# Kernel tuning notes

Hardware: AMD Instinct MI355X
Metric: run time of the kernel (lower is better)

## Reference

```python
import jax, jax.numpy as jnp
import numpy as np

N = 100000
E = 1600000
D_IN = 128
D_OUT = 128
BN_EPS = 1e-5


def setup_inputs() -> dict:
    key = jax.random.key(0)
    k_x, k_src, k_dst, k_val, k_w = jax.random.split(key, 5)
    x = jax.random.normal(k_x, (N, D_IN), dtype=jnp.float32)
    edge_src = jax.random.randint(k_src, (E,), 0, N, dtype=jnp.int64)
    edge_dst = jax.random.randint(k_dst, (E,), 0, N, dtype=jnp.int64)
    edge_vals = jax.random.uniform(k_val, (E,), dtype=jnp.float32)
    # kaiming-uniform-like init for weight
    bound = float(np.sqrt(6.0 / D_IN))
    weight = jax.random.uniform(k_w, (D_IN, D_OUT), dtype=jnp.float32,
                                minval=-bound, maxval=bound)
    bias = jnp.zeros((D_OUT,), dtype=jnp.float32)
    gamma = jnp.ones((D_OUT,), dtype=jnp.float32)   # BatchNorm weight
    beta = jnp.zeros((D_OUT,), dtype=jnp.float32)   # BatchNorm bias
    return {"x": x, "edge_src": edge_src, "edge_dst": edge_dst,
            "edge_vals": edge_vals, "weight": weight, "bias": bias,
            "gamma": gamma, "beta": beta}


def reference(x, edge_src, edge_dst, edge_vals, weight, bias, gamma, beta):
    # SpMM: out[dst] += val * x[src]  (adj @ x with adj in COO form)
    msgs = x[edge_src] * edge_vals[:, None]            # [E, D_IN]
    agg = jax.ops.segment_sum(msgs, edge_dst, num_segments=N)  # [N, D_IN]
    # Dense linear
    h = jnp.dot(agg, weight) + bias                     # [N, D_OUT]
    # BatchNorm1d (training mode: batch statistics, biased variance)
    mean = jnp.mean(h, axis=0)
    var = jnp.mean(jnp.square(h - mean), axis=0)
    h_norm = (h - mean) * jax.lax.rsqrt(var + BN_EPS)
    return h_norm * gamma + beta
```

## Files before the change

### kernel.cpp

```cpp
#include <hip/hip_runtime.h>
#include <math.h>

#define D 128
#define BSHIFT 9
#define BROWS 512
#define TILE 8192
constexpr float BN_EPS = 1e-5f;
typedef unsigned long long ull;

__device__ __forceinline__ unsigned f2bf_rne(float f) {
    unsigned u = __float_as_uint(f);
    return (u + 0x7FFFu + ((u >> 16) & 1u)) >> 16;
}
__device__ __forceinline__ float bf_lo(unsigned u) { return __uint_as_float(u << 16); }
__device__ __forceinline__ float bf_hi(unsigned u) { return __uint_as_float(u & 0xFFFF0000u); }

__global__ __launch_bounds__(256) void phase1_kernel(
    const float* __restrict__ A,
    const float* __restrict__ W,
    unsigned* __restrict__ yb,
    int n,
    const int* __restrict__ esrc, const int* __restrict__ edst,
    const float* __restrict__ evals,
    uint2* __restrict__ slices,
    int* __restrict__ ofs_t,
    int B, int nwgA, int E)
{
    __shared__ __align__(16) char smem[81920];
    const int tid = threadIdx.x;

    if ((int)blockIdx.x < nwgA) {
        int* h   = (int*)smem;
        int* ps  = h + 256;
        int* cur = ps + 256;
        const int wg = blockIdx.x;
        const int e0 = wg * TILE;
        const int e1 = min(e0 + TILE, E);

        h[tid] = 0;
        __syncthreads();
        for (int e = e0 + tid; e < e1; e += 256)
            atomicAdd(&h[edst[e] >> BSHIFT], 1);
        __syncthreads();

        const int v = h[tid];
        ps[tid] = v;
        __syncthreads();
        for (int off = 1; off < 256; off <<= 1) {
            int t = (tid >= off) ? ps[tid - off] : 0;
            __syncthreads();
            if (tid >= off) ps[tid] += t;
            __syncthreads();
        }
        const int excl = ps[tid] - v;
        if (tid < B) {
            cur[tid] = excl;
            ofs_t[(size_t)tid * nwgA + wg] = excl;
        }
        if (tid == 0) ofs_t[(size_t)B * nwgA + wg] = e1 - e0;
        __syncthreads();

        uint2* slice = slices + (size_t)wg * TILE;
        for (int e = e0 + tid; e < e1; e += 256) {
            int d = edst[e];
            int b = d >> BSHIFT;
            int p = atomicAdd(&cur[b], 1);
            uint2 rec;
            rec.x = (unsigned)(d & (BROWS - 1)) | ((unsigned)esrc[e] << BSHIFT);
            rec.y = __float_as_uint(evals[e]);
            slice[p] = rec;
        }
    } else {
        float* sW = (float*)smem;
        float (*sA)[128] = (float(*)[128])(smem + 65536);

        const float4* W4  = (const float4*)W;
        float4*       sW4 = (float4*)sW;
#pragma unroll
        for (int i = 0; i < 16; i++) sW4[tid + 256 * i] = W4[tid + 256 * i];

        const int row0 = (blockIdx.x - nwgA) * 32;
        const float4* A4  = (const float4*)(A + (size_t)row0 * D);
        float4*       sA4 = (float4*)&sA[0][0];
#pragma unroll
        for (int i = 0; i < 4; i++) {
            int idx = tid + 256 * i;
            sA4[idx] = ((size_t)row0 * D + (size_t)idx * 4 < (size_t)n * D)
                           ? A4[idx] : make_float4(0.f, 0.f, 0.f, 0.f);
        }
        __syncthreads();

        const int tx = tid & 31;
        const int ty = tid >> 5;
        const int c0 = tx * 4;

        float acc[4][4] = {};
        for (int k0 = 0; k0 < 128; k0 += 4) {
            float4 a[4];
#pragma unroll
            for (int j = 0; j < 4; j++)
                a[j] = *(const float4*)&sA[ty + 8 * j][k0];
#pragma unroll
            for (int kk = 0; kk < 4; kk++) {
                const float4 w = *(const float4*)&sW[(k0 + kk) * 128 + c0];
                const float ak[4] = { kk == 0 ? a[0].x : kk == 1 ? a[0].y : kk == 2 ? a[0].z : a[0].w,
                                      kk == 0 ? a[1].x : kk == 1 ? a[1].y : kk == 2 ? a[1].z : a[1].w,
                                      kk == 0 ? a[2].x : kk == 1 ? a[2].y : kk == 2 ? a[2].z : a[2].w,
                                      kk == 0 ? a[3].x : kk == 1 ? a[3].y : kk == 2 ? a[3].z : a[3].w };
#pragma unroll
                for (int j = 0; j < 4; j++) {
                    acc[j][0] += ak[j] * w.x;
                    acc[j][1] += ak[j] * w.y;
                    acc[j][2] += ak[j] * w.z;
                    acc[j][3] += ak[j] * w.w;
                }
            }
        }

#pragma unroll
        for (int j = 0; j < 4; j++) {
            const int row = row0 + ty + 8 * j;
            if (row < n) {
                uint2 o;
                o.x = f2bf_rne(acc[j][0]) | (f2bf_rne(acc[j][1]) << 16);
                o.y = f2bf_rne(acc[j][2]) | (f2bf_rne(acc[j][3]) << 16);
                ((uint2*)(yb + (size_t)row * 64))[tx] = o;
            }
        }
    }
}

__global__ __launch_bounds__(1024) void binB_kernel(
    const uint2* __restrict__ slices,
    const int* __restrict__ ofs_t,
    int* __restrict__ rowptr,
    ull* __restrict__ csr,
    int B, int nwgA, int n)
{
    __shared__ int srow[256];
    __shared__ int erow[256];
    __shared__ int red[256];
    __shared__ int hist[BROWS];
    __shared__ int curs[BROWS];
    __shared__ int ps[BROWS];
    __shared__ int s_bbase;

    const int tid  = threadIdx.x;
    const int b    = blockIdx.x;
    const int w    = tid >> 6;
    const int lane = tid & 63;

    for (int i = tid; i < nwgA; i += 1024) {
        srow[i] = ofs_t[(size_t)b * nwgA + i];
        erow[i] = ofs_t[(size_t)(b + 1) * nwgA + i];
    }
    if (tid < BROWS) hist[tid] = 0;
    __syncthreads();

    if (tid < 256) red[tid] = (tid < nwgA) ? srow[tid] : 0;
    __syncthreads();
    for (int off = 128; off > 0; off >>= 1) {
        if (tid < off) red[tid] += red[tid + off];
        __syncthreads();
    }
    if (tid == 0) s_bbase = red[0];
    __syncthreads();

    for (int wg = w; wg < nwgA; wg += 16) {
        const int s = srow[wg];
        const int e = erow[wg];
        const uint2* run = slices + (size_t)wg * TILE;
        for (int i = s + lane; i < e; i += 64)
            atomicAdd(&hist[run[i].x & (BROWS - 1)], 1);
    }
    __syncthreads();

    int v0 = 0;
    if (tid < BROWS) { v0 = hist[tid]; ps[tid] = v0; }
    __syncthreads();
    for (int off = 1; off < BROWS; off <<= 1) {
        int t = 0;
        if (tid < BROWS && tid >= off) t = ps[tid - off];
        __syncthreads();
        if (tid < BROWS) ps[tid] += t;
        __syncthreads();
    }
    if (tid < BROWS) {
        const int excl = s_bbase + ps[tid] - v0;
        curs[tid] = excl;
        const int r = (b << BSHIFT) + tid;
        if (r < n) rowptr[r] = excl + v0;
    }
    __syncthreads();

    for (int wg = w; wg < nwgA; wg += 16) {
        const int s = srow[wg];
        const int e = erow[wg];
        const uint2* run = slices + (size_t)wg * TILE;
        for (int i = s + lane; i < e; i += 64) {
            uint2 r = run[i];
            int pos = atomicAdd(&curs[r.x & (BROWS - 1)], 1);
            csr[pos] = ((ull)r.y << 32) | (r.x >> BSHIFT);
        }
    }
}

__global__ __launch_bounds__(256) void spmm_stats_kernel(
    const unsigned* __restrict__ yb,
    const int* __restrict__ rowptr,
    const ull* __restrict__ csr,
    float* __restrict__ h,
    float* __restrict__ stats,
    int n)
{
    __shared__ int   rp[65];
    __shared__ float ssum[128];
    __shared__ float ssq[128];

    const int tid       = threadIdx.x;
    const int blockRow0 = blockIdx.x * 64;

    if (tid < 128) { ssum[tid] = 0.f; ssq[tid] = 0.f; }
    if (tid < 65) {
        int idx = blockRow0 + tid - 1;
        rp[tid] = (idx < 0) ? 0 : rowptr[min(idx, n - 1)];
    }
    __syncthreads();

    const int wv    = tid >> 6;
    const int lane  = tid & 63;
    const int half  = lane >> 5;
    const int li    = lane & 31;
    const int rbase = blockRow0 + wv * 16;

    float s0 = 0.f, s1 = 0.f, s2 = 0.f, s3 = 0.f;
    float q0 = 0.f, q1 = 0.f, q2 = 0.f, q3 = 0.f;

    if (rbase < n) {
        const int r1 = min(rbase + 16, n);

        int curRow  = rbase;
        int eNext   = rp[curRow - blockRow0];
        int eRowEnd = rp[curRow - blockRow0 + 1];
        int accRow  = rbase;
        float a0 = 0.f, a1 = 0.f, a2 = 0.f, a3 = 0.f;

        auto flushTo = [&](int newRow) {
            float t0 = a0 + __shfl_down(a0, 32);
            float t1 = a1 + __shfl_down(a1, 32);
            float t2 = a2 + __shfl_down(a2, 32);
            float t3 = a3 + __shfl_down(a3, 32);
            if (lane < 32) {
                *(float4*)&h[(size_t)accRow * D + li * 4] =
                    make_float4(t0, t1, t2, t3);
                s0 += t0; s1 += t1; s2 += t2; s3 += t3;
                q0 += t0 * t0; q1 += t1 * t1; q2 += t2 * t2; q3 += t3 * t3;
            }
            a0 = a1 = a2 = a3 = 0.f;
            for (int z = accRow + 1; z < newRow; ++z)
                if (lane < 32)
                    *(float4*)&h[(size_t)z * D + li * 4] =
                        make_float4(0.f, 0.f, 0.f, 0.f);
            accRow = newRow;
        };

        auto build = [&](ull (&c)[8], unsigned& ridPack, unsigned& vmask) -> int {
            int cnt = 0; ridPack = 0u; vmask = 0u;
            bool done = false;
#pragma unroll
            for (int j = 0; j < 8; ++j) {
                if (!done) {
                    while (eNext >= eRowEnd) {
                        if (curRow + 1 >= r1) { done = true; break; }
                        ++curRow;
                        eNext   = rp[curRow - blockRow0];
                        eRowEnd = rp[curRow - blockRow0 + 1];
                    }
                    if (!done) {
                        ridPack |= (unsigned)(curRow - rbase) << (4 * j);
                        int  ei    = eNext + half;
                        bool valid = ei < eRowEnd;
                        int  ci    = valid ? ei : (eRowEnd - 1);
                        c[j] = csr[ci];
                        vmask |= (valid ? 1u : 0u) << j;
                        eNext += 2;
                        ++cnt;
                    }
                }
            }
            return cnt;
        };

        uint2 u[8];
        auto gather = [&](const ull (&c)[8], int cnt) {
#pragma unroll
            for (int j = 0; j < 8; ++j)
                if (j < cnt)
                    u[j] = *(const uint2*)(yb + (size_t)(unsigned)c[j] * 64 + 2 * li);
        };
        auto fmaChunk = [&](const ull (&c)[8], unsigned ridPack, unsigned vmask,
                            int cnt) {
#pragma unroll
            for (int j = 0; j < 8; ++j) {
                if (j < cnt) {
                    int r = rbase + (int)((ridPack >> (4 * j)) & 15u);
                    if (r != accRow) flushTo(r);
                    float v = ((vmask >> j) & 1u)
                                  ? __uint_as_float((unsigned)(c[j] >> 32))
                                  : 0.f;
                    a0 += v * bf_lo(u[j].x);
                    a1 += v * bf_hi(u[j].x);
                    a2 += v * bf_lo(u[j].y);
                    a3 += v * bf_hi(u[j].y);
                }
            }
        };

        ull cA[8], cB[8];
        unsigned ridA, vmA, ridB, vmB;
        int cntA = build(cA, ridA, vmA);
        while (cntA > 0) {
            gather(cA, cntA);
            int cntB = build(cB, ridB, vmB);
            fmaChunk(cA, ridA, vmA, cntA);
            if (cntB == 0) break;
            gather(cB, cntB);
            cntA = build(cA, ridA, vmA);
            fmaChunk(cB, ridB, vmB, cntB);
        }
        flushTo(r1);
    }

    if (rbase < n && lane < 32) {
        atomicAdd(&ssum[4 * li + 0], s0); atomicAdd(&ssum[4 * li + 1], s1);
        atomicAdd(&ssum[4 * li + 2], s2); atomicAdd(&ssum[4 * li + 3], s3);
        atomicAdd(&ssq [4 * li + 0], q0); atomicAdd(&ssq [4 * li + 1], q1);
        atomicAdd(&ssq [4 * li + 2], q2); atomicAdd(&ssq [4 * li + 3], q3);
    }
    __syncthreads();
    if (tid < 128) {
        atomicAdd(&stats[tid],       ssum[tid]);
        atomicAdd(&stats[128 + tid], ssq[tid]);
    }
}

__global__ __launch_bounds__(256) void bn_apply_kernel(
    float* __restrict__ h,
    const float* __restrict__ stats,
    const float* __restrict__ gamma,
    const float* __restrict__ beta,
    int n)
{
    __shared__ float s_scale[128];
    __shared__ float s_shift[128];
    const int tid = threadIdx.x;
    if (tid < 128) {
        const float invn = 1.0f / (float)n;
        const float mean = stats[tid] * invn;
        const float var  = stats[128 + tid] * invn - mean * mean;
        const float inv  = rsqrtf(var + BN_EPS);
        const float g    = gamma[tid] * inv;
        s_scale[tid] = g;
        s_shift[tid] = beta[tid] - mean * g;
    }
    __syncthreads();

    float4* h4 = (float4*)h;
    const size_t total = (size_t)n * D / 4;
    const size_t stride = (size_t)gridDim.x * blockDim.x;
    for (size_t i = (size_t)blockIdx.x * blockDim.x + tid; i < total; i += stride) {
        float4 v = h4[i];
        const int c = (int)((i * 4) & (D - 1));
        v.x = v.x * s_scale[c]     + s_shift[c];
        v.y = v.y * s_scale[c + 1] + s_shift[c + 1];
        v.z = v.z * s_scale[c + 2] + s_shift[c + 2];
        v.w = v.w * s_scale[c + 3] + s_shift[c + 3];
        h4[i] = v;
    }
}

__global__ __launch_bounds__(256) void spmm_atomic_kernel(
    const float* __restrict__ x,
    const int* __restrict__ esrc, const int* __restrict__ edst,
    const float* __restrict__ eval, float* __restrict__ agg, int E)
{
    int wave  = (blockIdx.x * blockDim.x + threadIdx.x) >> 6;
    int lane  = threadIdx.x & 63;
    int nwave = (gridDim.x * blockDim.x) >> 6;
    for (int e = wave; e < E; e += nwave) {
        int   s = esrc[e];
        int   d = edst[e];
        float v = eval[e];
        const float2 xv = ((const float2*)(x + (size_t)s * D))[lane];
        float* ar = agg + (size_t)d * D + lane * 2;
        atomicAdd(ar,     xv.x * v);
        atomicAdd(ar + 1, xv.y * v);
    }
}

__global__ __launch_bounds__(256) void gemm_stats_kernel(
    const float* __restrict__ A,
    const float* __restrict__ W,
    float* __restrict__ h,
    float* __restrict__ stats,
    int n)
{
    __shared__ float sW[128 * 128];
    __shared__ float sA[32][128];
    const int tid = threadIdx.x;
    const float4* W4  = (const float4*)W;
    float4*       sW4 = (float4*)sW;
#pragma unroll
    for (int i = 0; i < 16; i++) sW4[tid + 256 * i] = W4[tid + 256 * i];
    const int row0 = blockIdx.x * 32;
    const float4* A4  = (const float4*)(A + (size_t)row0 * D);
    float4*       sA4 = (float4*)&sA[0][0];
#pragma unroll
    for (int i = 0; i < 4; i++) {
        int idx = tid + 256 * i;
        sA4[idx] = ((size_t)row0 * D + (size_t)idx * 4 < (size_t)n * D)
                       ? A4[idx] : make_float4(0.f, 0.f, 0.f, 0.f);
    }
    __syncthreads();
    const int tx = tid & 31, ty = tid >> 5, c0 = tx * 4;
    float acc[4][4] = {};
    for (int k = 0; k < 128; k++) {
        const float4 w = *(const float4*)&sW[k * 128 + c0];
#pragma unroll
        for (int j = 0; j < 4; j++) {
            const float a = sA[ty + 8 * j][k];
            acc[j][0] += a * w.x; acc[j][1] += a * w.y;
            acc[j][2] += a * w.z; acc[j][3] += a * w.w;
        }
    }
#pragma unroll
    for (int j = 0; j < 4; j++) {
        const int row = row0 + ty + 8 * j;
        if (row < n)
            *(float4*)&h[(size_t)row * D + c0] =
                make_float4(acc[j][0], acc[j][1], acc[j][2], acc[j][3]);
    }
    __syncthreads();
    float* csum = &sA[0][0];
    float* csq  = csum + 128;
    if (tid < 128) { csum[tid] = 0.f; csq[tid] = 0.f; }
    __syncthreads();
#pragma unroll
    for (int c = 0; c < 4; c++) {
        float s = 0.f, q = 0.f;
#pragma unroll
        for (int j = 0; j < 4; j++) { s += acc[j][c]; q += acc[j][c] * acc[j][c]; }
        atomicAdd(&csum[c0 + c], s);
        atomicAdd(&csq[c0 + c], q);
    }
    __syncthreads();
    if (tid < 128) {
        atomicAdd(&stats[tid],       csum[tid]);
        atomicAdd(&stats[128 + tid], csq[tid]);
    }
}

extern "C" void kernel_launch(void* const* d_in, const int* in_sizes, int n_in,
                              void* d_out, int out_size, void* d_ws, size_t ws_size,
                              hipStream_t stream)
{
    const float* x     = (const float*)d_in[0];
    const int*   esrc  = (const int*)d_in[1];
    const int*   edst  = (const int*)d_in[2];
    const float* evals = (const float*)d_in[3];
    const float* W     = (const float*)d_in[4];
    const float* gamma = (const float*)d_in[6];
    const float* beta  = (const float*)d_in[7];
    float* out = (float*)d_out;

    const int n = in_sizes[0] / D;
    const int E = in_sizes[1];

    const int B     = (n + BROWS - 1) >> BSHIFT;
    const int nwgA  = (E + TILE - 1) / TILE;
    const int ngemm = (n + 31) / 32;

    unsigned* yb     = (unsigned*)d_ws;
    float*    stats  = (float*)(yb + (size_t)n * 64);
    int*      ofs_t  = (int*)(stats + 256);
    int*      rowptr = ofs_t + (size_t)(B + 1) * nwgA;
    size_t    w_off  = (size_t)n * 64 + 256 + (size_t)(B + 1) * nwgA + n;
    w_off += (w_off & 1);
    uint2*    slices = (uint2*)((unsigned*)d_ws + w_off);
    ull*      csr    = (ull*)(slices + (size_t)nwgA * TILE);
    const size_t need = (w_off + (size_t)nwgA * TILE * 2 + (size_t)E * 2) * 4;

    if (ws_size >= need && B <= 256 && nwgA <= 256) {
        hipMemsetAsync(stats, 0, 256 * 4, stream);
        phase1_kernel<<<nwgA + ngemm, 256, 0, stream>>>(
            x, W, yb, n, esrc, edst, evals, slices, ofs_t, B, nwgA, E);
        binB_kernel<<<B, 1024, 0, stream>>>(
            slices, ofs_t, rowptr, csr, B, nwgA, n);
        spmm_stats_kernel<<<(n + 63) / 64, 256, 0, stream>>>(
            yb, rowptr, csr, out, stats, n);
        bn_apply_kernel<<<2048, 256, 0, stream>>>(out, stats, gamma, beta, n);
    } else {
        float* agg = (float*)d_ws;
        float* st  = agg + (size_t)n * D;
        hipMemsetAsync(d_ws, 0, ((size_t)n * D + 256) * 4, stream);
        spmm_atomic_kernel<<<4096, 256, 0, stream>>>(x, esrc, edst, evals, agg, E);
        gemm_stats_kernel<<<(n + 31) / 32, 256, 0, stream>>>(agg, W, out, st, n);
        bn_apply_kernel<<<2048, 256, 0, stream>>>(out, st, gamma, beta, n);
    }
}
```

Baseline: 311.3 us.

## Assign one row per half-wave in SpMM instead of splitting edges across halves

The SpMM+stats kernel now processes two rows at a time per wave, one per 32-lane half, looping over each row's edges in chunks of 8 with padded loads. This replaces the old scheme where both halves shared one row's edges and rows were switched mid-chunk with shuffle-reduce flushes. It removes the per-edge row bookkeeping, branchy flush logic and cross-half shuffles. In exchange, load imbalance between the paired rows leaves lanes idle, and there is no longer software pipelining of gathers across chunks.

After: 309.0 us. No clear change (-0.7%).

```diff
diff --git a/kernel.cpp b/kernel.cpp
--- a/kernel.cpp
+++ b/kernel.cpp
@@ -219,6 +219,11 @@
 
     const int tid       = threadIdx.x;
     const int blockRow0 = blockIdx.x * 64;
+    const int wv        = tid >> 6;
+    const int lane      = tid & 63;
+    const int half      = lane >> 5;
+    const int li        = lane & 31;
+    const int rbase     = blockRow0 + wv * 16;
 
     if (tid < 128) { ssum[tid] = 0.f; ssq[tid] = 0.f; }
     if (tid < 65) {
@@ -227,111 +232,52 @@
     }
     __syncthreads();
 
-    const int wv    = tid >> 6;
-    const int lane  = tid & 63;
-    const int half  = lane >> 5;
-    const int li    = lane & 31;
-    const int rbase = blockRow0 + wv * 16;
-
     float s0 = 0.f, s1 = 0.f, s2 = 0.f, s3 = 0.f;
     float q0 = 0.f, q1 = 0.f, q2 = 0.f, q3 = 0.f;
 
     if (rbase < n) {
-        const int r1 = min(rbase + 16, n);
-
-        int curRow  = rbase;
-        int eNext   = rp[curRow - blockRow0];
-        int eRowEnd = rp[curRow - blockRow0 + 1];
-        int accRow  = rbase;
-        float a0 = 0.f, a1 = 0.f, a2 = 0.f, a3 = 0.f;
-
-        auto flushTo = [&](int newRow) {
-            float t0 = a0 + __shfl_down(a0, 32);
-            float t1 = a1 + __shfl_down(a1, 32);
-            float t2 = a2 + __shfl_down(a2, 32);
-            float t3 = a3 + __shfl_down(a3, 32);
-            if (lane < 32) {
-                *(float4*)&h[(size_t)accRow * D + li * 4] =
-                    make_float4(t0, t1, t2, t3);
-                s0 += t0; s1 += t1; s2 += t2; s3 += t3;
-                q0 += t0 * t0; q1 += t1 * t1; q2 += t2 * t2; q3 += t3 * t3;
-            }
-            a0 = a1 = a2 = a3 = 0.f;
-            for (int z = accRow + 1; z < newRow; ++z)
-                if (lane < 32)
-                    *(float4*)&h[(size_t)z * D + li * 4] =
-                        make_float4(0.f, 0.f, 0.f, 0.f);
-            accRow = newRow;
-        };
-
-        auto build = [&](ull (&c)[8], unsigned& ridPack, unsigned& vmask) -> int {
-            int cnt = 0; ridPack = 0u; vmask = 0u;
-            bool done = false;
-#pragma unroll
-            for (int j = 0; j < 8; ++j) {
-                if (!done) {
-                    while (eNext >= eRowEnd) {
-                        if (curRow + 1 >= r1) { done = true; break; }
-                        ++curRow;
-                        eNext   = rp[curRow - blockRow0];
-                        eRowEnd = rp[curRow - blockRow0 + 1];
-                    }
-                    if (!done) {
-                        ridPack |= (unsigned)(curRow - rbase) << (4 * j);
-                        int  ei    = eNext + half;
-                        bool valid = ei < eRowEnd;
-                        int  ci    = valid ? ei : (eRowEnd - 1);
-                        c[j] = csr[ci];
-                        vmask |= (valid ? 1u : 0u) << j;
-                        eNext += 2;
-                        ++cnt;
-                    }
+        for (int pr = 0; pr < 16; pr += 2) {
+            const int  rA    = rbase + pr + half;
+            const bool rowOK = rA < n;
+            const int  s_    = rowOK ? rp[rA - blockRow0]     : 0;
+            const int  e_    = rowOK ? rp[rA - blockRow0 + 1] : 0;
+            const int  nA    = e_ - s_;
+            const int  nMax  = max(nA, __shfl_xor(nA, 32));
+
+            float a0 = 0.f, a1 = 0.f, a2 = 0.f, a3 = 0.f;
+            for (int i = 0; i < nMax; i += 8) {
+                ull cd[8];
+#pragma unroll
+                for (int j = 0; j < 8; j++) {
+                    int idx = s_ + i + j;
+                    int ce  = (idx < e_) ? idx : (nA ? e_ - 1 : 0);
+                    cd[j] = csr[ce];
+                }
+                uint2 u[8];
+                float v[8];
+#pragma unroll
+                for (int j = 0; j < 8; j++) {
+                    u[j] = *(const uint2*)(yb + (size_t)(unsigned)cd[j] * 64 + 2 * li);
+                    v[j] = (s_ + i + j < e_)
+                               ? __uint_as_float((unsigned)(cd[j] >> 32))
+                               : 0.f;
+                }
+#pragma unroll
+                for (int j = 0; j < 8; j++) {
+                    a0 += v[j] * bf_lo(u[j].x);
+                    a1 += v[j] * bf_hi(u[j].x);
+                    a2 += v[j] * bf_lo(u[j].y);
+                    a3 += v[j] * bf_hi(u[j].y);
                 }
             }
-            return cnt;
-        };
-
-        uint2 u[8];
-        auto gather = [&](const ull (&c)[8], int cnt) {
-#pragma unroll
-            for (int j = 0; j < 8; ++j)
-                if (j < cnt)
-                    u[j] = *(const uint2*)(yb + (size_t)(unsigned)c[j] * 64 + 2 * li);
-        };
-        auto fmaChunk = [&](const ull (&c)[8], unsigned ridPack, unsigned vmask,
-                            int cnt) {
-#pragma unroll
-            for (int j = 0; j < 8; ++j) {
-                if (j < cnt) {
-                    int r = rbase + (int)((ridPack >> (4 * j)) & 15u);
-                    if (r != accRow) flushTo(r);
-                    float v = ((vmask >> j) & 1u)
-                                  ? __uint_as_float((unsigned)(c[j] >> 32))
-                                  : 0.f;
-                    a0 += v * bf_lo(u[j].x);
-                    a1 += v * bf_hi(u[j].x);
-                    a2 += v * bf_lo(u[j].y);
-                    a3 += v * bf_hi(u[j].y);
-                }
+
+            if (rowOK) {
+                *(float4*)&h[(size_t)rA * D + 4 * li] = make_float4(a0, a1, a2, a3);
+                s0 += a0; s1 += a1; s2 += a2; s3 += a3;
+                q0 += a0 * a0; q1 += a1 * a1; q2 += a2 * a2; q3 += a3 * a3;
             }
-        };
-
-        ull cA[8], cB[8];
-        unsigned ridA, vmA, ridB, vmB;
-        int cntA = build(cA, ridA, vmA);
-        while (cntA > 0) {
-            gather(cA, cntA);
-            int cntB = build(cB, ridB, vmB);
-            fmaChunk(cA, ridA, vmA, cntA);
-            if (cntB == 0) break;
-            gather(cB, cntB);
-            cntA = build(cA, ridA, vmA);
-            fmaChunk(cB, ridB, vmB, cntB);
-        }
-        flushTo(r1);
-    }
-
-    if (rbase < n && lane < 32) {
+        }
+
         atomicAdd(&ssum[4 * li + 0], s0); atomicAdd(&ssum[4 * li + 1], s1);
         atomicAdd(&ssum[4 * li + 2], s2); atomicAdd(&ssum[4 * li + 3], s3);
         atomicAdd(&ssq [4 * li + 0], q0); atomicAdd(&ssq [4 * li + 1], q1);
```
